# Optimization experiments

Hardware: AMD Instinct MI355X
Metric: run time of the kernel (lower is better)

The kernel has to match this reference:

```python
import jax, jax.numpy as jnp
import numpy as np

POOL = 7        # pool_size
NUM_ROIS = 128  # num_rois
WINDOW = 4      # window_size


def setup_inputs() -> dict:
    key = jax.random.key(0)
    k1, k2 = jax.random.split(key)
    img = jax.random.normal(k1, (16, 28, 28, 512), dtype=jnp.float32)
    rois = jax.random.uniform(k2, (16, NUM_ROIS * 5), dtype=jnp.float32)
    return {"img": img, "rois": rois}


def _crop_and_resize(image, boxes, crop):
    """tf.image.crop_and_resize (bilinear, extrapolation_value=0) on a single image.
    image: (H, W, C); boxes: (N, 4) normalized (y1, x1, y2, x2). Returns (N, crop, crop, C)."""
    H, W, C = image.shape
    dt = image.dtype
    y1, x1, y2, x2 = boxes[:, 0], boxes[:, 1], boxes[:, 2], boxes[:, 3]
    i = jnp.arange(crop, dtype=dt)
    # sample grid (crop > 1 branch of TF crop_and_resize)
    ys = y1[:, None] * (H - 1) + i[None, :] * ((y2 - y1) * (H - 1) / (crop - 1))[:, None]  # (N, crop)
    xs = x1[:, None] * (W - 1) + i[None, :] * ((x2 - x1) * (W - 1) / (crop - 1))[:, None]  # (N, crop)
    y0f = jnp.floor(ys)
    x0f = jnp.floor(xs)
    ly = ys - y0f  # fractional weights
    lx = xs - x0f
    y0 = jnp.clip(y0f, 0, H - 1).astype(jnp.int32)
    y1i = jnp.clip(y0f + 1, 0, H - 1).astype(jnp.int32)
    x0 = jnp.clip(x0f, 0, W - 1).astype(jnp.int32)
    x1i = jnp.clip(x0f + 1, 0, W - 1).astype(jnp.int32)
    g = lambda yi, xi: image[yi[:, :, None], xi[:, None, :], :]  # (N, crop, crop, C) gather
    tl, tr, bl, br = g(y0, x0), g(y0, x1i), g(y1i, x0), g(y1i, x1i)
    lxb = lx[:, None, :, None]
    lyb = ly[:, :, None, None]
    val = (tl + (tr - tl) * lxb) * (1 - lyb) + (bl + (br - bl) * lxb) * lyb
    # out-of-range samples -> extrapolation_value = 0
    vy = (ys >= 0) & (ys <= H - 1)
    vx = (xs >= 0) & (xs <= W - 1)
    mask = (vy[:, :, None, None] & vx[:, None, :, None]).astype(dt)
    return val * mask


def reference(img, rois):
    B, H, W, C = img.shape  # H=W=28, C=512 per the layer's hardcoded reshape
    r = rois.reshape(-1, 5)[:, 3:]  # (B*num_rois, 2): columns 3,4 -> x1, y1
    x1 = r[:, 0]
    y1 = r[:, 1]
    x2 = x1 + WINDOW / W  # window_size / cols
    y2 = y1 + WINDOW / H  # window_size / rows
    boxes = jnp.stack([y1, x1, y2, x2], axis=-1)  # (B*num_rois, 4)
    # Original tiles img num_rois times but sets box_ind = zeros, so every crop
    # samples from batch element 0's feature map. Reproduce that exactly.
    crops = _crop_and_resize(img[0], boxes, POOL)  # (B*num_rois, POOL, POOL, C)
    return crops.reshape(B, POOL, POOL, NUM_ROIS * C)
```

## Files before the change

### kernel.cpp

```cpp
#include <hip/hip_runtime.h>

#define POOLSZ 7
#define IMG_H  28
#define IMG_W  28
#define IMG_C  512
#define C4     128
#define HALF4  64
#define PATCH  6
#define NPIX   (PATCH * PATCH)
#define TOT_ROIS 2048

typedef float f4 __attribute__((ext_vector_type(4)));

__global__ __launch_bounds__(256, 4)
void roi_crop_resize_v3(const float* __restrict__ img,
                        const float* __restrict__ rois,
                        float* __restrict__ out) {
    __shared__ f4 patch[NPIX * HALF4];

    int n    = blockIdx.x >> 1;
    int half = blockIdx.x & 1;

    float x1 = rois[n * 5 + 3];
    float y1 = rois[n * 5 + 4];
    float x2 = x1 + 4.0f / 28.0f;
    float y2 = y1 + 4.0f / 28.0f;
    const float Hm1 = 27.0f, Wm1 = 27.0f;
    float dy  = (y2 - y1) * Hm1 / 6.0f;
    float dx  = (x2 - x1) * Wm1 / 6.0f;
    float ys0 = y1 * Hm1;
    float xs0 = x1 * Wm1;

    int Y0 = (int)floorf(ys0); if (Y0 > 27) Y0 = 27; if (Y0 < 0) Y0 = 0;
    int X0 = (int)floorf(xs0); if (X0 > 27) X0 = 27; if (X0 < 0) X0 = 0;

    const f4* img4 = (const f4*)img;
    int tid   = threadIdx.x;
    int cbase = half * HALF4;

    for (int i = tid; i < NPIX * HALF4; i += 256) {
        int c   = i & (HALF4 - 1);
        int pix = i >> 6;
        int ry  = Y0 + pix / PATCH; if (ry > 27) ry = 27;
        int rx  = X0 + pix % PATCH; if (rx > 27) rx = 27;
        patch[i] = img4[(ry * IMG_W + rx) * C4 + cbase + c];
    }
    __syncthreads();

    f4* out4 = (f4*)out + n * 49 * C4 + cbase;
    for (int i = tid; i < 49 * HALF4; i += 256) {
        int c = i & (HALF4 - 1);
        int p = i >> 6;
        int py = p / POOLSZ, px = p % POOLSZ;

        float ys = ys0 + (float)py * dy;
        float xs = xs0 + (float)px * dx;
        float y0f = floorf(ys), x0f = floorf(xs);
        float ly = ys - y0f, lx = xs - x0f;
        int y0  = (int)fminf(fmaxf(y0f,       0.f), Hm1);
        int y1i = (int)fminf(fmaxf(y0f + 1.f, 0.f), Hm1);
        int x0  = (int)fminf(fmaxf(x0f,       0.f), Wm1);
        int x1i = (int)fminf(fmaxf(x0f + 1.f, 0.f), Wm1);
        float m = ((ys >= 0.f) & (ys <= Hm1) & (xs >= 0.f) & (xs <= Wm1)) ? 1.f : 0.f;

        int ry0 = y0  - Y0, ry1 = y1i - Y0;
        int rx0 = x0  - X0, rx1 = x1i - X0;
        f4 tl = patch[(ry0 * PATCH + rx0) * HALF4 + c];
        f4 tr = patch[(ry0 * PATCH + rx1) * HALF4 + c];
        f4 bl = patch[(ry1 * PATCH + rx0) * HALF4 + c];
        f4 br = patch[(ry1 * PATCH + rx1) * HALF4 + c];

        float omly = 1.f - ly;
        f4 v = ((tl + (tr - tl) * lx) * omly + (bl + (br - bl) * lx) * ly) * m;

        out4[p * C4 + c] = v;
    }
}

extern "C" void kernel_launch(void* const* d_in, const int* in_sizes, int n_in,
                              void* d_out, int out_size, void* d_ws, size_t ws_size,
                              hipStream_t stream) {
    const float* img  = (const float*)d_in[0];
    const float* rois = (const float*)d_in[1];
    float* out = (float*)d_out;

    roi_crop_resize_v3<<<TOT_ROIS * 2, 256, 0, stream>>>(img, rois, out);
}
```

Baseline: 213.0 us.

## Drop shared-memory patch staging and gather bilinear corners directly from global

Removes the shared-memory staging of a 6x6 pixel patch and the barrier. Each thread now reads its four bilinear corner values straight from the image in global memory and relies on the L1/L2 caches, since the whole 1.6MB image of batch 0 fits in cache. Blocks now cover all 512 channels of one ROI instead of half, which halves the grid, and launch bounds are raised to 8 blocks per CU. The cost is more global load instructions per output (four cached loads instead of one staged load), in exchange for no LDS traffic and no synchronization.

```diff
diff --git a/kernel.cpp b/kernel.cpp
--- a/kernel.cpp
+++ b/kernel.cpp
@@ -5,21 +5,16 @@
 #define IMG_W  28
 #define IMG_C  512
 #define C4     128
-#define HALF4  64
-#define PATCH  6
-#define NPIX   (PATCH * PATCH)
 #define TOT_ROIS 2048
 
 typedef float f4 __attribute__((ext_vector_type(4)));
 
-__global__ __launch_bounds__(256, 4)
-void roi_crop_resize_v3(const float* __restrict__ img,
+__global__ __launch_bounds__(256, 8)
+void roi_crop_resize_v4(const float* __restrict__ img,
                         const float* __restrict__ rois,
                         float* __restrict__ out) {
-    __shared__ f4 patch[NPIX * HALF4];
-
-    int n    = blockIdx.x >> 1;
-    int half = blockIdx.x & 1;
+    int n   = blockIdx.x;
+    int tid = threadIdx.x;
 
     float x1 = rois[n * 5 + 3];
     float y1 = rois[n * 5 + 4];
@@ -31,26 +26,12 @@
     float ys0 = y1 * Hm1;
     float xs0 = x1 * Wm1;
 
-    int Y0 = (int)floorf(ys0); if (Y0 > 27) Y0 = 27; if (Y0 < 0) Y0 = 0;
-    int X0 = (int)floorf(xs0); if (X0 > 27) X0 = 27; if (X0 < 0) X0 = 0;
+    const f4* img4 = (const f4*)img;
+    f4* out4 = (f4*)out + n * 49 * C4;
 
-    const f4* img4 = (const f4*)img;
-    int tid   = threadIdx.x;
-    int cbase = half * HALF4;
-
-    for (int i = tid; i < NPIX * HALF4; i += 256) {
-        int c   = i & (HALF4 - 1);
-        int pix = i >> 6;
-        int ry  = Y0 + pix / PATCH; if (ry > 27) ry = 27;
-        int rx  = X0 + pix % PATCH; if (rx > 27) rx = 27;
-        patch[i] = img4[(ry * IMG_W + rx) * C4 + cbase + c];
-    }
-    __syncthreads();
-
-    f4* out4 = (f4*)out + n * 49 * C4 + cbase;
-    for (int i = tid; i < 49 * HALF4; i += 256) {
-        int c = i & (HALF4 - 1);
-        int p = i >> 6;
+    for (int i = tid; i < 49 * C4; i += 256) {
+        int c = i & (C4 - 1);
+        int p = i >> 7;
         int py = p / POOLSZ, px = p % POOLSZ;
 
         float ys = ys0 + (float)py * dy;
@@ -63,12 +44,10 @@
         int x1i = (int)fminf(fmaxf(x0f + 1.f, 0.f), Wm1);
         float m = ((ys >= 0.f) & (ys <= Hm1) & (xs >= 0.f) & (xs <= Wm1)) ? 1.f : 0.f;
 
-        int ry0 = y0  - Y0, ry1 = y1i - Y0;
-        int rx0 = x0  - X0, rx1 = x1i - X0;
-        f4 tl = patch[(ry0 * PATCH + rx0) * HALF4 + c];
-        f4 tr = patch[(ry0 * PATCH + rx1) * HALF4 + c];
-        f4 bl = patch[(ry1 * PATCH + rx0) * HALF4 + c];
-        f4 br = patch[(ry1 * PATCH + rx1) * HALF4 + c];
+        f4 tl = img4[(y0  * IMG_W + x0 ) * C4 + c];
+        f4 tr = img4[(y0  * IMG_W + x1i) * C4 + c];
+        f4 bl = img4[(y1i * IMG_W + x0 ) * C4 + c];
+        f4 br = img4[(y1i * IMG_W + x1i) * C4 + c];
 
         float omly = 1.f - ly;
         f4 v = ((tl + (tr - tl) * lx) * omly + (bl + (br - bl) * lx) * ly) * m;
@@ -84,5 +63,5 @@
     const float* rois = (const float*)d_in[1];
     float* out = (float*)d_out;
 
-    roi_crop_resize_v3<<<TOT_ROIS * 2, 256, 0, stream>>>(img, rois, out);
+    roi_crop_resize_v4<<<TOT_ROIS, 256, 0, stream>>>(img, rois, out);
 }
```

Result: no change. 213.0 us (+0.0%).
